# Optimization experiments

Hardware: AMD Instinct MI355X
Metric: run time of the kernel (lower is better)

The kernel has to match this reference:

```python
import jax, jax.numpy as jnp
import numpy as np
from jax import lax

B, CHI, CHO, H, W = 8, 128, 128, 64, 64
K = 3
KK = K * K


def setup_inputs() -> dict:
    key = jax.random.key(0)
    ks = jax.random.split(key, 7)
    x = jax.random.normal(ks[0], (B, CHI, H, W), jnp.float32)
    # small offset-conv weights so sampled offsets stay in a realistic few-pixel range
    off_w = jax.random.normal(ks[1], (3 * KK, CHI, K, K), jnp.float32) * 0.01
    off_b = jnp.zeros((3 * KK,), jnp.float32)
    w = jax.random.normal(ks[2], (CHO, CHI, K, K), jnp.float32) / np.sqrt(CHI * KK).astype(np.float32)
    b = jnp.zeros((CHO,), jnp.float32)
    gamma = jax.random.uniform(ks[3], (CHO,), jnp.float32)  # nn.init.uniform_ on BN weight
    beta = jnp.zeros((CHO,), jnp.float32)
    return {"x": x, "off_w": off_w, "off_b": off_b, "w": w, "b": b, "gamma": gamma, "beta": beta}


def _deform_conv(x, off_w, off_b, w, b):
    """DCNv2 modulated deformable conv, k=3, stride=1, pad=1, dil=1, 1 deform group."""
    B_, C, H_, W_ = x.shape
    # offset/mask branch: plain 3x3 conv -> 27 channels (2*9 offsets, 9 masks)
    om = lax.conv_general_dilated(x, off_w, (1, 1), ((1, 1), (1, 1)),
                                  dimension_numbers=("NCHW", "OIHW", "NCHW"))
    om = om + off_b[None, :, None, None]
    off = om[:, : 2 * KK].reshape(B_, KK, 2, H_, W_)  # [B,9,2,H,W]; ch 2k=y, 2k+1=x
    mask = jax.nn.sigmoid(om[:, 2 * KK:])             # [B,9,H,W]

    ky, kx = jnp.meshgrid(jnp.arange(K, dtype=jnp.float32),
                          jnp.arange(K, dtype=jnp.float32), indexing="ij")
    ky = ky.reshape(KK); kx = kx.reshape(KK)
    # sampling positions: p = p0 - pad + k*dil + offset
    py = off[:, :, 0] + (jnp.arange(H_, dtype=jnp.float32) - 1.0)[None, None, :, None] + ky[None, :, None, None]
    px = off[:, :, 1] + (jnp.arange(W_, dtype=jnp.float32) - 1.0)[None, None, None, :] + kx[None, :, None, None]

    y0 = jnp.floor(py); x0 = jnp.floor(px)
    ly = py - y0; lx = px - x0
    xf = x.reshape(B_, C, H_ * W_)

    def corner(yi, xi, wgt):
        valid = ((yi >= 0) & (yi <= H_ - 1) & (xi >= 0) & (xi <= W_ - 1)).astype(x.dtype)
        yc = jnp.clip(yi, 0, H_ - 1).astype(jnp.int32)
        xc = jnp.clip(xi, 0, W_ - 1).astype(jnp.int32)
        idx = (yc * W_ + xc).reshape(B_, KK * H_ * W_)
        g = jax.vmap(lambda xb, ib: xb[:, ib])(xf, idx).reshape(B_, C, KK, H_, W_)
        return g * (valid * wgt)[:, None]

    val = (corner(y0, x0, (1 - ly) * (1 - lx))
           + corner(y0, x0 + 1, (1 - ly) * lx)
           + corner(y0 + 1, x0, ly * (1 - lx))
           + corner(y0 + 1, x0 + 1, ly * lx))  # [B,C,9,H,W]
    val = val * mask[:, None]  # modulation
    out = jnp.einsum("bckhw,ock->bohw", val, w.reshape(w.shape[0], C, KK))
    return out + b[None, :, None, None]


def reference(x, off_w, off_b, w, b, gamma, beta):
    y = _deform_conv(x, off_w, off_b, w, b)
    # BatchNorm2d in training mode (batch statistics), eps=1e-5, then ReLU
    mean = y.mean(axis=(0, 2, 3))
    var = y.var(axis=(0, 2, 3))
    yn = (y - mean[None, :, None, None]) * lax.rsqrt(var[None, :, None, None] + 1e-5)
    return jax.nn.relu(yn * gamma[None, :, None, None] + beta[None, :, None, None])
```

## Files before the change

### kernel.cpp

```cpp
#include <hip/hip_runtime.h>
#include <hip/hip_bf16.h>
#include <math.h>

#define HH 64
#define WW 64
#define HW 4096
#define LDV 136

typedef __bf16 bf16x8 __attribute__((ext_vector_type(8)));
typedef float floatx4 __attribute__((ext_vector_type(4)));
typedef unsigned int uint4a __attribute__((ext_vector_type(4)));

#define WS_Y    0u
#define WS_PSQ  16777216u
#define WS_XTB  16778240u
#define WS_WTB  25166848u
#define WS_OWB  25461760u

static __device__ inline ushort f2bf(float f) {
  __hip_bfloat16 h = __float2bfloat16(f);
  return __builtin_bit_cast(ushort, h);
}
static __device__ inline float lo16(unsigned int u) { return __builtin_bit_cast(float, u << 16); }
static __device__ inline float hi16(unsigned int u) { return __builtin_bit_cast(float, u & 0xffff0000u); }

__global__ __launch_bounds__(256) void k_prepw(const float* __restrict__ w,
                                               const float* __restrict__ ow,
                                               ushort* __restrict__ wtb,
                                               ushort* __restrict__ owb) {
  int idx = blockIdx.x * 256 + threadIdx.x;
  if (idx < 147456) {
    int c = idx & 127, o = (idx >> 7) & 127, k = idx >> 14;
    wtb[idx] = f2bf(w[(o * 128 + c) * 9 + k]);
  } else {
    int j = idx - 147456;
    if (j < 36864) {
      int c = j & 127, o = (j >> 7) & 31, k = j >> 12;
      float v = (o < 27) ? ow[(o * 128 + c) * 9 + k] : 0.f;
      owb[j] = f2bf(v);
    }
  }
}

__global__ __launch_bounds__(256) void k_xt(const float* __restrict__ x,
                                            ushort* __restrict__ xtb) {
  __shared__ float tile[32][33];
  int hw0 = blockIdx.x * 32;
  int c0 = blockIdx.y * 32;
  int b = blockIdx.z;
  int col = threadIdx.x & 31, row = threadIdx.x >> 5;
  const float* xb = x + ((size_t)b * 128 + c0) * HW + hw0;
#pragma unroll
  for (int i = 0; i < 32; i += 8)
    tile[row + i][col] = xb[(size_t)(row + i) * HW + col];
  __syncthreads();
  int cpair = threadIdx.x & 15, hwi = threadIdx.x >> 4;
  ushort* xo = xtb + ((size_t)b * HW + hw0) * 128 + c0;
#pragma unroll
  for (int i = 0; i < 32; i += 16) {
    int hw = hwi + i;
    unsigned int v = (unsigned int)f2bf(tile[2 * cpair][hw]) |
                     ((unsigned int)f2bf(tile[2 * cpair + 1][hw]) << 16);
    *(unsigned int*)(&xo[(size_t)hw * 128 + 2 * cpair]) = v;
  }
}

__global__ __launch_bounds__(256) void k_main(
    const ushort* __restrict__ xtb, const ushort* __restrict__ wtb,
    const ushort* __restrict__ owb, const float* __restrict__ off_b,
    const float* __restrict__ bias, float* __restrict__ y) {
  __shared__ ushort Vl[32 * LDV];
  __shared__ float omL[27 * 32];
  int t = threadIdx.x;
  int lane = t & 63, wv = t >> 6;
  int li = lane & 15, quad = lane >> 4;
  int hr = blockIdx.x;
  int row = hr >> 1, p0b = (hr & 1) * 32;
  int b = blockIdx.y;
  const ushort* xb = xtb + (size_t)b * HW * 128;
  int sp = t & 31, scg = t >> 5;
  int gp = p0b + sp;

  int mi = wv & 1, ni = wv >> 1;
  floatx4 oacc = (floatx4){0.f, 0.f, 0.f, 0.f};
  uint4a u0, u1;
  {
    int ry = row - 1, cx = gp - 1;
    bool v = (ry >= 0 && cx >= 0);
    int idx = v ? (ry * WW + cx) : 0;
    const uint4a* src = (const uint4a*)(xb + (size_t)idx * 128 + scg * 16);
    uint4a a0 = src[0], a1 = src[1];
    u0 = v ? a0 : (uint4a){0u, 0u, 0u, 0u};
    u1 = v ? a1 : (uint4a){0u, 0u, 0u, 0u};
  }
  for (int k = 0; k < 9; ++k) {
    __syncthreads();
    *(uint4a*)(&Vl[sp * LDV + scg * 16]) = u0;
    *(uint4a*)(&Vl[sp * LDV + scg * 16 + 8]) = u1;
    if (k < 8) {
      int kk = k + 1;
      int ky = kk / 3, kx = kk % 3;
      int ry = row - 1 + ky, cx = gp - 1 + kx;
      bool v = (ry >= 0 && ry < HH && cx >= 0 && cx < WW);
      int idx = v ? (ry * WW + cx) : 0;
      const uint4a* src = (const uint4a*)(xb + (size_t)idx * 128 + scg * 16);
      uint4a a0 = src[0], a1 = src[1];
      u0 = v ? a0 : (uint4a){0u, 0u, 0u, 0u};
      u1 = v ? a1 : (uint4a){0u, 0u, 0u, 0u};
    }
    __syncthreads();
#pragma unroll
    for (int ks = 0; ks < 4; ++ks) {
      bf16x8 bfrag = __builtin_bit_cast(bf16x8,
          *(const uint4a*)(&Vl[(ni * 16 + li) * LDV + ks * 32 + quad * 8]));
      bf16x8 afrag = __builtin_bit_cast(bf16x8,
          *(const uint4a*)(&owb[(size_t)(k * 32 + mi * 16 + li) * 128 + ks * 32 + quad * 8]));
      oacc = __builtin_amdgcn_mfma_f32_16x16x32_bf16(afrag, bfrag, oacc, 0, 0, 0);
    }
  }
#pragma unroll
  for (int r = 0; r < 4; ++r) {
    int o = mi * 16 + quad * 4 + r;
    if (o < 27) omL[o * 32 + ni * 16 + li] = oacc[r] + off_b[o];
  }
  __syncthreads();

  floatx4 macc[2][2];
#pragma unroll
  for (int i = 0; i < 2; ++i)
#pragma unroll
    for (int j = 0; j < 2; ++j) macc[i][j] = (floatx4){0.f, 0.f, 0.f, 0.f};

  float wq[4];
  int idx4[4];
  uint4a u[8];

  auto prep = [&](int k) {
    int ky = k / 3, kx = k % 3;
    float offy = omL[(2 * k) * 32 + sp];
    float offx = omL[(2 * k + 1) * 32 + sp];
    float mraw = omL[(18 + k) * 32 + sp];
    float m = 1.f / (1.f + __expf(-mraw));
    float py = offy + (float)(row - 1 + ky);
    float px = offx + (float)(gp - 1 + kx);
    float y0f = floorf(py), x0f = floorf(px);
    float ly = py - y0f, lx = px - x0f;
    int iy0 = (int)y0f, ix0 = (int)x0f;
    int iy1 = iy0 + 1, ix1 = ix0 + 1;
    float w00 = (1.f - ly) * (1.f - lx) * m, w01 = (1.f - ly) * lx * m;
    float w10 = ly * (1.f - lx) * m, w11 = ly * lx * m;
    if (iy0 < 0 || iy0 > HH - 1) { w00 = 0.f; w01 = 0.f; }
    if (iy1 < 0 || iy1 > HH - 1) { w10 = 0.f; w11 = 0.f; }
    if (ix0 < 0 || ix0 > WW - 1) { w00 = 0.f; w10 = 0.f; }
    if (ix1 < 0 || ix1 > WW - 1) { w01 = 0.f; w11 = 0.f; }
    int cy0 = min(max(iy0, 0), HH - 1), cy1 = min(max(iy1, 0), HH - 1);
    int cx0 = min(max(ix0, 0), WW - 1), cx1 = min(max(ix1, 0), WW - 1);
    idx4[0] = cy0 * WW + cx0;
    idx4[1] = cy0 * WW + cx1;
    idx4[2] = cy1 * WW + cx0;
    idx4[3] = cy1 * WW + cx1;
    wq[0] = w00; wq[1] = w01; wq[2] = w10; wq[3] = w11;
  };
  auto issue = [&]() {
#pragma unroll
    for (int c = 0; c < 4; ++c) {
      const uint4a* s = (const uint4a*)(xb + (size_t)idx4[c] * 128 + scg * 16);
      u[c * 2] = s[0];
      u[c * 2 + 1] = s[1];
    }
  };

  prep(0);
  issue();
  for (int k = 0; k < 9; ++k) {
    __syncthreads();
#pragma unroll
    for (int j = 0; j < 2; ++j) {
      uint4a outv;
#pragma unroll
      for (int e = 0; e < 4; ++e) {
        float rlo = wq[0] * lo16(u[0 + j][e]) + wq[1] * lo16(u[2 + j][e]) +
                    wq[2] * lo16(u[4 + j][e]) + wq[3] * lo16(u[6 + j][e]);
        float rhi = wq[0] * hi16(u[0 + j][e]) + wq[1] * hi16(u[2 + j][e]) +
                    wq[2] * hi16(u[4 + j][e]) + wq[3] * hi16(u[6 + j][e]);
        outv[e] = (unsigned int)f2bf(rlo) | ((unsigned int)f2bf(rhi) << 16);
      }
      *(uint4a*)(&Vl[sp * LDV + scg * 16 + j * 8]) = outv;
    }
    if (k < 8) {
      prep(k + 1);
      issue();
    }
    __syncthreads();
    const ushort* Arow = &wtb[(size_t)(k * 128 + wv * 32) * 128];
#pragma unroll
    for (int ks = 0; ks < 4; ++ks) {
      bf16x8 b0 = __builtin_bit_cast(bf16x8,
          *(const uint4a*)(&Vl[(li)*LDV + ks * 32 + quad * 8]));
      bf16x8 b1 = __builtin_bit_cast(bf16x8,
          *(const uint4a*)(&Vl[(16 + li) * LDV + ks * 32 + quad * 8]));
      bf16x8 a0 = __builtin_bit_cast(bf16x8,
          *(const uint4a*)(Arow + (size_t)(li)*128 + ks * 32 + quad * 8));
      bf16x8 a1 = __builtin_bit_cast(bf16x8,
          *(const uint4a*)(Arow + (size_t)(16 + li) * 128 + ks * 32 + quad * 8));
      macc[0][0] = __builtin_amdgcn_mfma_f32_16x16x32_bf16(a0, b0, macc[0][0], 0, 0, 0);
      macc[0][1] = __builtin_amdgcn_mfma_f32_16x16x32_bf16(a0, b1, macc[0][1], 0, 0, 0);
      macc[1][0] = __builtin_amdgcn_mfma_f32_16x16x32_bf16(a1, b0, macc[1][0], 0, 0, 0);
      macc[1][1] = __builtin_amdgcn_mfma_f32_16x16x32_bf16(a1, b1, macc[1][1], 0, 0, 0);
    }
  }
#pragma unroll
  for (int ot = 0; ot < 2; ++ot)
#pragma unroll
    for (int pt = 0; pt < 2; ++pt)
#pragma unroll
      for (int r = 0; r < 4; ++r) {
        int o = wv * 32 + ot * 16 + quad * 4 + r;
        int p = p0b + pt * 16 + li;
        y[((size_t)(b * 128 + o)) * HW + row * 64 + p] = macc[ot][pt][r] + bias[o];
      }
}

__global__ __launch_bounds__(256) void k_stats(const float* __restrict__ y,
                                               float* __restrict__ psq) {
  int o = blockIdx.x, b = blockIdx.y, t = threadIdx.x;
  const float4* yb = (const float4*)(y + ((size_t)(b * 128 + o)) * HW);
  float s = 0.f, q = 0.f;
#pragma unroll
  for (int i = 0; i < 4; ++i) {
    float4 v = yb[t + i * 256];
    s += v.x + v.y + v.z + v.w;
    q += v.x * v.x + v.y * v.y + v.z * v.z + v.w * v.w;
  }
#pragma unroll
  for (int off = 32; off >= 1; off >>= 1) {
    s += __shfl_down(s, off, 64);
    q += __shfl_down(q, off, 64);
  }
  __shared__ float bs[4], bq[4];
  if ((t & 63) == 0) { bs[t >> 6] = s; bq[t >> 6] = q; }
  __syncthreads();
  if (t == 0) {
    atomicAdd(&psq[o], bs[0] + bs[1] + bs[2] + bs[3]);
    atomicAdd(&psq[128 + o], bq[0] + bq[1] + bq[2] + bq[3]);
  }
}

__global__ __launch_bounds__(256) void k_norm(const float* __restrict__ y,
                                              const float* __restrict__ psq,
                                              const float* __restrict__ gamma,
                                              const float* __restrict__ beta,
                                              float* __restrict__ out) {
  int blk = blockIdx.x;
  int o = (blk >> 2) & 127;
  float s = psq[o], q = psq[128 + o];
  float mean = s * (1.f / 32768.f);
  float var = q * (1.f / 32768.f) - mean * mean;
  float scale = gamma[o] * rsqrtf(var + 1e-5f);
  float shift = beta[o] - mean * scale;
  int i4 = blk * 256 + threadIdx.x;
  float4 v = ((const float4*)y)[i4];
  float4 r;
  r.x = fmaxf(v.x * scale + shift, 0.f);
  r.y = fmaxf(v.y * scale + shift, 0.f);
  r.z = fmaxf(v.z * scale + shift, 0.f);
  r.w = fmaxf(v.w * scale + shift, 0.f);
  ((float4*)out)[i4] = r;
}

extern "C" void kernel_launch(void* const* d_in, const int* in_sizes, int n_in,
                              void* d_out, int out_size, void* d_ws, size_t ws_size,
                              hipStream_t stream) {
  const float* x     = (const float*)d_in[0];
  const float* off_w = (const float*)d_in[1];
  const float* off_b = (const float*)d_in[2];
  const float* w     = (const float*)d_in[3];
  const float* bias  = (const float*)d_in[4];
  const float* gamma = (const float*)d_in[5];
  const float* beta  = (const float*)d_in[6];
  float* out = (float*)d_out;
  char* ws = (char*)d_ws;

  float* y    = (float*)(ws + WS_Y);
  float* psq  = (float*)(ws + WS_PSQ);
  ushort* xtb = (ushort*)(ws + WS_XTB);
  ushort* wtb = (ushort*)(ws + WS_WTB);
  ushort* owb = (ushort*)(ws + WS_OWB);

  hipMemsetAsync(psq, 0, 256 * sizeof(float), stream);
  k_prepw<<<720, 256, 0, stream>>>(w, off_w, wtb, owb);
  k_xt<<<dim3(128, 4, 8), 256, 0, stream>>>(x, xtb);
  k_main<<<dim3(128, 8), 256, 0, stream>>>(xtb, wtb, owb, off_b, bias, y);
  k_stats<<<dim3(128, 8), 256, 0, stream>>>(y, psq);
  k_norm<<<4096, 256, 0, stream>>>(y, psq, gamma, beta, out);
}
```

Measured before the change: 185.1 us.

## Remap gather threads so 16 lanes cover one pixel's channels for coalescing

```diff
diff --git a/kernel.cpp b/kernel.cpp
--- a/kernel.cpp
+++ b/kernel.cpp
@@ -10,6 +10,7 @@
 typedef __bf16 bf16x8 __attribute__((ext_vector_type(8)));
 typedef float floatx4 __attribute__((ext_vector_type(4)));
 typedef unsigned int uint4a __attribute__((ext_vector_type(4)));
+typedef unsigned int uint2a __attribute__((ext_vector_type(2)));
 
 #define WS_Y    0u
 #define WS_PSQ  16777216u
@@ -54,15 +55,14 @@
   for (int i = 0; i < 32; i += 8)
     tile[row + i][col] = xb[(size_t)(row + i) * HW + col];
   __syncthreads();
-  int cpair = threadIdx.x & 15, hwi = threadIdx.x >> 4;
+  int hw = threadIdx.x >> 3, cq = threadIdx.x & 7;
   ushort* xo = xtb + ((size_t)b * HW + hw0) * 128 + c0;
-#pragma unroll
-  for (int i = 0; i < 32; i += 16) {
-    int hw = hwi + i;
-    unsigned int v = (unsigned int)f2bf(tile[2 * cpair][hw]) |
-                     ((unsigned int)f2bf(tile[2 * cpair + 1][hw]) << 16);
-    *(unsigned int*)(&xo[(size_t)hw * 128 + 2 * cpair]) = v;
-  }
+  unsigned int lo = (unsigned int)f2bf(tile[cq * 4 + 0][hw]) |
+                    ((unsigned int)f2bf(tile[cq * 4 + 1][hw]) << 16);
+  unsigned int hi = (unsigned int)f2bf(tile[cq * 4 + 2][hw]) |
+                    ((unsigned int)f2bf(tile[cq * 4 + 3][hw]) << 16);
+  uint2a v2 = (uint2a){lo, hi};
+  *(uint2a*)(&xo[(size_t)hw * 128 + cq * 4]) = v2;
 }
 
 __global__ __launch_bounds__(256) void k_main(
@@ -78,35 +78,29 @@
   int row = hr >> 1, p0b = (hr & 1) * 32;
   int b = blockIdx.y;
   const ushort* xb = xtb + (size_t)b * HW * 128;
-  int sp = t & 31, scg = t >> 5;
-  int gp = p0b + sp;
+  int ch = t & 15;
+  int pq = t >> 4;
 
   int mi = wv & 1, ni = wv >> 1;
   floatx4 oacc = (floatx4){0.f, 0.f, 0.f, 0.f};
   uint4a u0, u1;
-  {
-    int ry = row - 1, cx = gp - 1;
-    bool v = (ry >= 0 && cx >= 0);
+  auto p1load = [&](int k, int p, uint4a& u) {
+    int ky = k / 3, kx = k % 3;
+    int ry = row - 1 + ky, cx = p0b + p - 1 + kx;
+    bool v = (ry >= 0 && ry < HH && cx >= 0 && cx < WW);
     int idx = v ? (ry * WW + cx) : 0;
-    const uint4a* src = (const uint4a*)(xb + (size_t)idx * 128 + scg * 16);
-    uint4a a0 = src[0], a1 = src[1];
-    u0 = v ? a0 : (uint4a){0u, 0u, 0u, 0u};
-    u1 = v ? a1 : (uint4a){0u, 0u, 0u, 0u};
-  }
+    uint4a a = *(const uint4a*)(xb + (size_t)idx * 128 + ch * 8);
+    u = v ? a : (uint4a){0u, 0u, 0u, 0u};
+  };
+  p1load(0, pq, u0);
+  p1load(0, pq + 16, u1);
   for (int k = 0; k < 9; ++k) {
     __syncthreads();
-    *(uint4a*)(&Vl[sp * LDV + scg * 16]) = u0;
-    *(uint4a*)(&Vl[sp * LDV + scg * 16 + 8]) = u1;
+    *(uint4a*)(&Vl[pq * LDV + ch * 8]) = u0;
+    *(uint4a*)(&Vl[(pq + 16) * LDV + ch * 8]) = u1;
     if (k < 8) {
-      int kk = k + 1;
-      int ky = kk / 3, kx = kk % 3;
-      int ry = row - 1 + ky, cx = gp - 1 + kx;
-      bool v = (ry >= 0 && ry < HH && cx >= 0 && cx < WW);
-      int idx = v ? (ry * WW + cx) : 0;
-      const uint4a* src = (const uint4a*)(xb + (size_t)idx * 128 + scg * 16);
-      uint4a a0 = src[0], a1 = src[1];
-      u0 = v ? a0 : (uint4a){0u, 0u, 0u, 0u};
-      u1 = v ? a1 : (uint4a){0u, 0u, 0u, 0u};
+      p1load(k + 1, pq, u0);
+      p1load(k + 1, pq + 16, u1);
     }
     __syncthreads();
 #pragma unroll
@@ -131,18 +125,18 @@
 #pragma unroll
     for (int j = 0; j < 2; ++j) macc[i][j] = (floatx4){0.f, 0.f, 0.f, 0.f};
 
-  float wq[4];
-  int idx4[4];
+  float wqA[4], wqB[4];
+  int idxA[4], idxB[4];
   uint4a u[8];
 
-  auto prep = [&](int k) {
+  auto prep = [&](int k, int p, float* wq, int* idx4) {
     int ky = k / 3, kx = k % 3;
-    float offy = omL[(2 * k) * 32 + sp];
-    float offx = omL[(2 * k + 1) * 32 + sp];
-    float mraw = omL[(18 + k) * 32 + sp];
+    float offy = omL[(2 * k) * 32 + p];
+    float offx = omL[(2 * k + 1) * 32 + p];
+    float mraw = omL[(18 + k) * 32 + p];
     float m = 1.f / (1.f + __expf(-mraw));
     float py = offy + (float)(row - 1 + ky);
-    float px = offx + (float)(gp - 1 + kx);
+    float px = offx + (float)(p0b + p - 1 + kx);
     float y0f = floorf(py), x0f = floorf(px);
     float ly = py - y0f, lx = px - x0f;
     int iy0 = (int)y0f, ix0 = (int)x0f;
@@ -163,32 +157,45 @@
   };
   auto issue = [&]() {
 #pragma unroll
-    for (int c = 0; c < 4; ++c) {
-      const uint4a* s = (const uint4a*)(xb + (size_t)idx4[c] * 128 + scg * 16);
-      u[c * 2] = s[0];
-      u[c * 2 + 1] = s[1];
-    }
+    for (int c = 0; c < 4; ++c)
+      u[c] = *(const uint4a*)(xb + (size_t)idxA[c] * 128 + ch * 8);
+#pragma unroll
+    for (int c = 0; c < 4; ++c)
+      u[4 + c] = *(const uint4a*)(xb + (size_t)idxB[c] * 128 + ch * 8);
   };
 
-  prep(0);
+  prep(0, pq, wqA, idxA);
+  prep(0, pq + 16, wqB, idxB);
   issue();
   for (int k = 0; k < 9; ++k) {
     __syncthreads();
-#pragma unroll
-    for (int j = 0; j < 2; ++j) {
+    {
       uint4a outv;
 #pragma unroll
       for (int e = 0; e < 4; ++e) {
-        float rlo = wq[0] * lo16(u[0 + j][e]) + wq[1] * lo16(u[2 + j][e]) +
-                    wq[2] * lo16(u[4 + j][e]) + wq[3] * lo16(u[6 + j][e]);
-        float rhi = wq[0] * hi16(u[0 + j][e]) + wq[1] * hi16(u[2 + j][e]) +
-                    wq[2] * hi16(u[4 + j][e]) + wq[3] * hi16(u[6 + j][e]);
+        float rlo = wqA[0] * lo16(u[0][e]) + wqA[1] * lo16(u[1][e]) +
+                    wqA[2] * lo16(u[2][e]) + wqA[3] * lo16(u[3][e]);
+        float rhi = wqA[0] * hi16(u[0][e]) + wqA[1] * hi16(u[1][e]) +
+                    wqA[2] * hi16(u[2][e]) + wqA[3] * hi16(u[3][e]);
         outv[e] = (unsigned int)f2bf(rlo) | ((unsigned int)f2bf(rhi) << 16);
       }
-      *(uint4a*)(&Vl[sp * LDV + scg * 16 + j * 8]) = outv;
+      *(uint4a*)(&Vl[pq * LDV + ch * 8]) = outv;
+    }
+    {
+      uint4a outv;
+#pragma unroll
+      for (int e = 0; e < 4; ++e) {
+        float rlo = wqB[0] * lo16(u[4][e]) + wqB[1] * lo16(u[5][e]) +
+                    wqB[2] * lo16(u[6][e]) + wqB[3] * lo16(u[7][e]);
+        float rhi = wqB[0] * hi16(u[4][e]) + wqB[1] * hi16(u[5][e]) +
+                    wqB[2] * hi16(u[6][e]) + wqB[3] * hi16(u[7][e]);
+        outv[e] = (unsigned int)f2bf(rlo) | ((unsigned int)f2bf(rhi) << 16);
+      }
+      *(uint4a*)(&Vl[(pq + 16) * LDV + ch * 8]) = outv;
     }
     if (k < 8) {
-      prep(k + 1);
+      prep(k + 1, pq, wqA, idxA);
+      prep(k + 1, pq + 16, wqB, idxB);
       issue();
     }
     __syncthreads();
```

Result: faster. 161.1 us (-13.0%).
